# Optimization experiments

Measured on AMD Instinct MI355X. Metric: run time of the kernel, lower is better.

Reference implementation:

```python
import jax, jax.numpy as jnp
import numpy as np

T, B, I, H = 256, 128, 512, 1024

def setup_inputs() -> dict:
    key = jax.random.key(0)
    k1, k2, k3, k4, k5 = jax.random.split(key, 5)
    s_ih = 1.0 / np.sqrt(H)
    return {
        "x": jax.random.normal(k1, (T, B, I), dtype=jnp.float32),
        "hidden": jnp.zeros((B, H), dtype=jnp.float32),
        "W_ih": jax.random.uniform(k2, (H, I), jnp.float32, -s_ih, s_ih),
        "W_hh": jax.random.uniform(k3, (H, H), jnp.float32, -s_ih, s_ih),
        "b_ih": jax.random.uniform(k4, (H,), jnp.float32, -s_ih, s_ih),
        "b_hh": jax.random.uniform(k5, (H,), jnp.float32, -s_ih, s_ih),
    }

def reference(x, hidden, W_ih, W_hh, b_ih, b_hh):
    # Faithful to the source: forward() applies the RNNCell to the SAME
    # initial hidden at every timestep (hidden is never updated in the loop).
    # out[t] = relu(x[t] @ W_ih^T + b_ih + hidden @ W_hh^T + b_hh)
    h_term = hidden @ W_hh.T + b_hh          # (B, H), shared across time
    pre = jnp.einsum('tbi,hi->tbh', x, W_ih) + b_ih + h_term  # (T, B, H)
    out = jax.nn.relu(pre)
    return out, out[-1]
```

## Files before the change

### kernel.cpp

```cpp
#include <hip/hip_runtime.h>
#include <hip/hip_bf16.h>
#include <stdint.h>

#define T_DIM 256
#define B_DIM 128
#define I_DIM 512
#define H_DIM 1024
#define M_DIM (T_DIM * B_DIM)

typedef __attribute__((ext_vector_type(4))) float f32x4;
typedef __attribute__((ext_vector_type(8))) short short8;

__device__ inline unsigned short f2bf(float f) {
    __hip_bfloat16 h = __float2bfloat16(f);
    unsigned short u;
    __builtin_memcpy(&u, &h, sizeof(u));
    return u;
}

__device__ inline void gload_lds16(const void* g, void* l) {
    __builtin_amdgcn_global_load_lds(
        (const __attribute__((address_space(1))) uint32_t*)g,
        (__attribute__((address_space(3))) uint32_t*)l, 16, 0, 0);
}

__global__ void pack_W(const float* __restrict__ W, unsigned short* __restrict__ Wp) {
    int id = blockIdx.x * 256 + threadIdx.x;
    int s = id & 7;
    int r = (id >> 3) & 127;
    int kst = (id >> 10) & 7;
    int nt = id >> 13;
    int srcg = s ^ (r & 7);
    const float* src = W + (size_t)(nt * 128 + r) * I_DIM + kst * 64 + srcg * 8;
    f32x4 lo = *(const f32x4*)src;
    f32x4 hi = *(const f32x4*)(src + 4);
    union { unsigned short us[8]; short8 v; } pk;
#pragma unroll
    for (int j = 0; j < 4; ++j) { pk.us[j] = f2bf(lo[j]); pk.us[4 + j] = f2bf(hi[j]); }
    *(short8*)(Wp + (size_t)id * 8) = pk.v;
}

__global__ __launch_bounds__(256, 3) void gemm_main(
    const float* __restrict__ X, const unsigned short* __restrict__ Wp,
    const float* __restrict__ biasall, float* __restrict__ C,
    float* __restrict__ Clast) {
    __shared__ float Asf[128 * 64];
    __shared__ unsigned short Bsb[128 * 64];

    const int tid = threadIdx.x;
    const int lane = tid & 63;
    const int wid = tid >> 6;
    const int wr = wid >> 1, wc = wid & 1;
    const int llo = lane & 15, lhi = lane >> 4;

    const int orig = blockIdx.x;
    const int nwg = gridDim.x;
    const int wg = ((orig & 7) * (nwg >> 3)) + (orig >> 3);
    const int mt = wg >> 3;
    const int nt = wg & 7;
    const int m0 = mt * 128;
    const int n0 = nt * 128;

    const int arow_l = tid >> 4;
    const int csrc = (tid & 15) ^ arow_l;
    const float* Abase = X + (size_t)(m0 + arow_l) * I_DIM + csrc * 4;
    const unsigned short* Bbase = Wp + (size_t)nt * 8 * 8192 + (size_t)tid * 8;

    f32x4 acc[4][4] = {};

#pragma unroll
    for (int kst = 0; kst < I_DIM / 64; ++kst) {
        if (kst) __syncthreads();
        const float* asrc = Abase + kst * 64;
#pragma unroll
        for (int g = 0; g < 8; ++g)
            gload_lds16(asrc + (size_t)g * 16 * I_DIM,
                        (char*)Asf + (g * 256 + tid) * 16);
        const unsigned short* bsrc = Bbase + kst * 8192;
#pragma unroll
        for (int g = 0; g < 4; ++g)
            gload_lds16(bsrc + g * 2048, (char*)Bsb + (g * 256 + tid) * 16);
        __syncthreads();

#pragma unroll
        for (int ks = 0; ks < 2; ++ks) {
            short8 af[4], bfv[4];
#pragma unroll
            for (int mi = 0; mi < 4; ++mi) {
                int ar = wr * 64 + mi * 16 + llo;
                int g0 = ks * 8 + lhi * 2;
                f32x4 a0 = *(const f32x4*)&Asf[ar * 64 + ((g0 ^ (ar & 15)) << 2)];
                f32x4 a1 = *(const f32x4*)&Asf[ar * 64 + (((g0 + 1) ^ (ar & 15)) << 2)];
                union { unsigned short s[8]; short8 v; } pk;
#pragma unroll
                for (int j = 0; j < 4; ++j) {
                    pk.s[j] = f2bf(a0[j]);
                    pk.s[4 + j] = f2bf(a1[j]);
                }
                af[mi] = pk.v;
            }
#pragma unroll
            for (int ni = 0; ni < 4; ++ni) {
                int br = wc * 64 + ni * 16 + llo;
                int g = ks * 4 + lhi;
                bfv[ni] = *(const short8*)&Bsb[br * 64 + ((g ^ (br & 7)) << 3)];
            }
#pragma unroll
            for (int mi = 0; mi < 4; ++mi)
#pragma unroll
                for (int ni = 0; ni < 4; ++ni)
                    acc[mi][ni] = __builtin_amdgcn_mfma_f32_16x16x32_bf16(
                        af[mi], bfv[ni], acc[mi][ni], 0, 0, 0);
        }
    }

    const bool last_tile = (m0 == M_DIM - 128);
#pragma unroll
    for (int mi = 0; mi < 4; ++mi) {
#pragma unroll
        for (int ni = 0; ni < 4; ++ni) {
            int col = n0 + wc * 64 + ni * 16 + llo;
            int rowb = m0 + wr * 64 + mi * 16 + lhi * 4;
#pragma unroll
            for (int r = 0; r < 4; ++r) {
                int row = rowb + r;
                float v = acc[mi][ni][r] + biasall[(row & 127) * H_DIM + col];
                v = fmaxf(v, 0.0f);
                C[(size_t)row * H_DIM + col] = v;
                if (last_tile) Clast[(row & 127) * H_DIM + col] = v;
            }
        }
    }
}

template <int MODE>
__global__ __launch_bounds__(256, 2) void gemm_bt(
    const float* __restrict__ A, const float* __restrict__ Bm,
    int M, int N, int K,
    const float* __restrict__ bias0, const float* __restrict__ bias1,
    float* __restrict__ C, float* __restrict__ Clast) {
    __shared__ unsigned short As[128 * 64];
    __shared__ unsigned short Bs[128 * 64];

    const int tid = threadIdx.x;
    const int wid = tid >> 6;
    const int lane = tid & 63;
    const int wr = wid >> 1, wc = wid & 1;
    const int lhi = lane >> 4;
    const int llo = lane & 15;

    const int orig = blockIdx.x;
    const int nwg = gridDim.x;
    const int wg = (nwg > 8 && (nwg & 7) == 0)
                       ? ((orig & 7) * (nwg >> 3) + (orig >> 3))
                       : orig;
    const int m0 = (wg >> 3) * 128;
    const int n0 = (wg & 7) * 128;

    const int srow = tid >> 3;
    const int c8 = tid & 7;
    const int slot8 = (c8 ^ (srow & 7)) * 8;

    const float* Aptr = A + (size_t)(m0 + srow) * K + c8 * 8;
    const float* Bptr = Bm + (size_t)(n0 + srow) * K + c8 * 8;

    f32x4 pf[2][4][2];

    auto issue = [&](int k0) {
#pragma unroll
        for (int g = 0; g < 4; ++g) {
            const float* pa = Aptr + (size_t)g * 32 * K + k0;
            const float* pb = Bptr + (size_t)g * 32 * K + k0;
            pf[0][g][0] = *(const f32x4*)pa;
            pf[0][g][1] = *(const f32x4*)(pa + 4);
            pf[1][g][0] = *(const f32x4*)pb;
            pf[1][g][1] = *(const f32x4*)(pb + 4);
        }
    };
    auto write_lds = [&]() {
#pragma unroll
        for (int g = 0; g < 4; ++g) {
            union { unsigned short s[8]; short8 v; } pka, pkb;
#pragma unroll
            for (int j = 0; j < 4; ++j) {
                pka.s[j] = f2bf(pf[0][g][0][j]);
                pka.s[4 + j] = f2bf(pf[0][g][1][j]);
                pkb.s[j] = f2bf(pf[1][g][0][j]);
                pkb.s[4 + j] = f2bf(pf[1][g][1][j]);
            }
            *(short8*)&As[(srow + g * 32) * 64 + slot8] = pka.v;
            *(short8*)&Bs[(srow + g * 32) * 64 + slot8] = pkb.v;
        }
    };

    f32x4 acc[4][4] = {};

    auto compute = [&]() {
#pragma unroll
        for (int ks = 0; ks < 2; ++ks) {
            short8 af[4], bfr[4];
#pragma unroll
            for (int mi = 0; mi < 4; ++mi) {
                int ar = wr * 64 + mi * 16 + llo;
                int slot = ((ks << 2) + lhi) ^ (ar & 7);
                af[mi] = *(const short8*)&As[ar * 64 + slot * 8];
            }
#pragma unroll
            for (int ni = 0; ni < 4; ++ni) {
                int br = wc * 64 + ni * 16 + llo;
                int slot = ((ks << 2) + lhi) ^ (br & 7);
                bfr[ni] = *(const short8*)&Bs[br * 64 + slot * 8];
            }
#pragma unroll
            for (int mi = 0; mi < 4; ++mi)
#pragma unroll
                for (int ni = 0; ni < 4; ++ni)
                    acc[mi][ni] = __builtin_amdgcn_mfma_f32_16x16x32_bf16(
                        af[mi], bfr[ni], acc[mi][ni], 0, 0, 0);
        }
    };

    issue(0);
    write_lds();
    __syncthreads();
    for (int k0 = 64; k0 < K; k0 += 64) {
        issue(k0);
        compute();
        __syncthreads();
        write_lds();
        __syncthreads();
    }
    compute();

    const bool last_tile = (m0 == M - 128);
#pragma unroll
    for (int mi = 0; mi < 4; ++mi) {
#pragma unroll
        for (int ni = 0; ni < 4; ++ni) {
            int col = n0 + wc * 64 + ni * 16 + llo;
            int rowb = m0 + wr * 64 + mi * 16 + lhi * 4;
            if (MODE == 0) {
                float bsum = bias0[col] + bias1[col];
#pragma unroll
                for (int r = 0; r < 4; ++r)
                    C[(size_t)(rowb + r) * N + col] = acc[mi][ni][r] + bsum;
            } else {
#pragma unroll
                for (int r = 0; r < 4; ++r) {
                    int row = rowb + r;
                    float v = acc[mi][ni][r] + bias0[(row & 127) * N + col];
                    v = fmaxf(v, 0.0f);
                    C[(size_t)row * N + col] = v;
                    if (last_tile) Clast[(row & 127) * N + col] = v;
                }
            }
        }
    }
}

extern "C" void kernel_launch(void* const* d_in, const int* in_sizes, int n_in,
                              void* d_out, int out_size, void* d_ws, size_t ws_size,
                              hipStream_t stream) {
    const float* x = (const float*)d_in[0];
    const float* hidden = (const float*)d_in[1];
    const float* W_ih = (const float*)d_in[2];
    const float* W_hh = (const float*)d_in[3];
    const float* b_ih = (const float*)d_in[4];
    const float* b_hh = (const float*)d_in[5];

    float* out = (float*)d_out;
    float* out_last = out + (size_t)T_DIM * B_DIM * H_DIM;

    float* biasall = (float*)d_ws;
    unsigned short* Wp = (unsigned short*)((char*)d_ws + 512 * 1024);
    const size_t ws_need = 512 * 1024 + (size_t)H_DIM * I_DIM * 2;

    gemm_bt<0><<<dim3(H_DIM / 128), dim3(256), 0, stream>>>(
        hidden, W_hh, B_DIM, H_DIM, H_DIM, b_ih, b_hh, biasall, nullptr);

    if (ws_size >= ws_need) {
        pack_W<<<dim3(H_DIM * I_DIM / 8 / 256), dim3(256), 0, stream>>>(W_ih, Wp);
        gemm_main<<<dim3(M_DIM / 128 * (H_DIM / 128)), dim3(256), 0, stream>>>(
            x, Wp, biasall, out, out_last);
    } else {
        gemm_bt<1><<<dim3(M_DIM / 128 * (H_DIM / 128)), dim3(256), 0, stream>>>(
            x, W_ih, M_DIM, H_DIM, I_DIM, biasall, nullptr, out, out_last);
    }
}
```

Baseline: 109.9 us.

## Pre-pack X to swizzled bf16 and double-buffer LDS tiles in main GEMM

Adds a separate pass that converts the activation tensor x to bf16 in the same swizzled tile layout as the weights. The main GEMM then loads bf16 directly with no per-fragment fp32-to-bf16 conversion. The main loop now double-buffers A and B tiles in LDS, using explicit vmcnt waits and barriers so the next k-stage loads overlap compute. In exchange it adds a full extra read and write of x (about 32 MB in bf16) in a pre-pass, doubles LDS use, and lowers the launch-bounds occupancy hint from 3 to 2.

```diff
diff --git a/kernel.cpp b/kernel.cpp
--- a/kernel.cpp
+++ b/kernel.cpp
@@ -24,28 +24,29 @@
         (__attribute__((address_space(3))) uint32_t*)l, 16, 0, 0);
 }
 
-__global__ void pack_W(const float* __restrict__ W, unsigned short* __restrict__ Wp) {
+__global__ void pack_swz(const float* __restrict__ src,
+                         unsigned short* __restrict__ dst) {
     int id = blockIdx.x * 256 + threadIdx.x;
-    int s = id & 7;
-    int r = (id >> 3) & 127;
+    int slot = id & 7;
+    int row = (id >> 3) & 127;
     int kst = (id >> 10) & 7;
-    int nt = id >> 13;
-    int srcg = s ^ (r & 7);
-    const float* src = W + (size_t)(nt * 128 + r) * I_DIM + kst * 64 + srcg * 8;
-    f32x4 lo = *(const f32x4*)src;
-    f32x4 hi = *(const f32x4*)(src + 4);
+    int tile = id >> 13;
+    int g = slot ^ (row & 7);
+    const float* s = src + (size_t)(tile * 128 + row) * I_DIM + kst * 64 + g * 8;
+    f32x4 lo = *(const f32x4*)s;
+    f32x4 hi = *(const f32x4*)(s + 4);
     union { unsigned short us[8]; short8 v; } pk;
 #pragma unroll
     for (int j = 0; j < 4; ++j) { pk.us[j] = f2bf(lo[j]); pk.us[4 + j] = f2bf(hi[j]); }
-    *(short8*)(Wp + (size_t)id * 8) = pk.v;
-}
-
-__global__ __launch_bounds__(256, 3) void gemm_main(
-    const float* __restrict__ X, const unsigned short* __restrict__ Wp,
+    *(short8*)(dst + (size_t)id * 8) = pk.v;
+}
+
+__global__ __launch_bounds__(256, 2) void gemm_main(
+    const unsigned short* __restrict__ Xp, const unsigned short* __restrict__ Wp,
     const float* __restrict__ biasall, float* __restrict__ C,
     float* __restrict__ Clast) {
-    __shared__ float Asf[128 * 64];
-    __shared__ unsigned short Bsb[128 * 64];
+    __shared__ unsigned short As[2][128 * 64];
+    __shared__ unsigned short Bs[2][128 * 64];
 
     const int tid = threadIdx.x;
     const int lane = tid & 63;
@@ -54,56 +55,43 @@
     const int llo = lane & 15, lhi = lane >> 4;
 
     const int orig = blockIdx.x;
-    const int nwg = gridDim.x;
-    const int wg = ((orig & 7) * (nwg >> 3)) + (orig >> 3);
+    const int wg = ((orig & 7) * (2048 >> 3)) + (orig >> 3);
     const int mt = wg >> 3;
     const int nt = wg & 7;
     const int m0 = mt * 128;
     const int n0 = nt * 128;
 
-    const int arow_l = tid >> 4;
-    const int csrc = (tid & 15) ^ arow_l;
-    const float* Abase = X + (size_t)(m0 + arow_l) * I_DIM + csrc * 4;
-    const unsigned short* Bbase = Wp + (size_t)nt * 8 * 8192 + (size_t)tid * 8;
+    const unsigned short* Abase = Xp + (size_t)mt * 65536 + (size_t)tid * 8;
+    const unsigned short* Bbase = Wp + (size_t)nt * 65536 + (size_t)tid * 8;
+
+    auto stage = [&](int kst, int buf) {
+        const unsigned short* a = Abase + (size_t)kst * 8192;
+        const unsigned short* b = Bbase + (size_t)kst * 8192;
+#pragma unroll
+        for (int g = 0; g < 4; ++g)
+            gload_lds16(a + g * 2048, (char*)As[buf] + (g * 256 + tid) * 16);
+#pragma unroll
+        for (int g = 0; g < 4; ++g)
+            gload_lds16(b + g * 2048, (char*)Bs[buf] + (g * 256 + tid) * 16);
+    };
 
     f32x4 acc[4][4] = {};
 
-#pragma unroll
-    for (int kst = 0; kst < I_DIM / 64; ++kst) {
-        if (kst) __syncthreads();
-        const float* asrc = Abase + kst * 64;
-#pragma unroll
-        for (int g = 0; g < 8; ++g)
-            gload_lds16(asrc + (size_t)g * 16 * I_DIM,
-                        (char*)Asf + (g * 256 + tid) * 16);
-        const unsigned short* bsrc = Bbase + kst * 8192;
-#pragma unroll
-        for (int g = 0; g < 4; ++g)
-            gload_lds16(bsrc + g * 2048, (char*)Bsb + (g * 256 + tid) * 16);
-        __syncthreads();
-
+    auto compute = [&](int buf) {
 #pragma unroll
         for (int ks = 0; ks < 2; ++ks) {
             short8 af[4], bfv[4];
 #pragma unroll
             for (int mi = 0; mi < 4; ++mi) {
                 int ar = wr * 64 + mi * 16 + llo;
-                int g0 = ks * 8 + lhi * 2;
-                f32x4 a0 = *(const f32x4*)&Asf[ar * 64 + ((g0 ^ (ar & 15)) << 2)];
-                f32x4 a1 = *(const f32x4*)&Asf[ar * 64 + (((g0 + 1) ^ (ar & 15)) << 2)];
-                union { unsigned short s[8]; short8 v; } pk;
-#pragma unroll
-                for (int j = 0; j < 4; ++j) {
-                    pk.s[j] = f2bf(a0[j]);
-                    pk.s[4 + j] = f2bf(a1[j]);
-                }
-                af[mi] = pk.v;
+                int g = ks * 4 + lhi;
+                af[mi] = *(const short8*)&As[buf][ar * 64 + ((g ^ (ar & 7)) << 3)];
             }
 #pragma unroll
             for (int ni = 0; ni < 4; ++ni) {
                 int br = wc * 64 + ni * 16 + llo;
                 int g = ks * 4 + lhi;
-                bfv[ni] = *(const short8*)&Bsb[br * 64 + ((g ^ (br & 7)) << 3)];
+                bfv[ni] = *(const short8*)&Bs[buf][br * 64 + ((g ^ (br & 7)) << 3)];
             }
 #pragma unroll
             for (int mi = 0; mi < 4; ++mi)
@@ -112,6 +100,22 @@
                     acc[mi][ni] = __builtin_amdgcn_mfma_f32_16x16x32_bf16(
                         af[mi], bfv[ni], acc[mi][ni], 0, 0, 0);
         }
+    };
+
+    stage(0, 0);
+    stage(1, 1);
+#pragma unroll
+    for (int k = 0; k < 8; ++k) {
+        if (k < 7)
+            asm volatile("s_waitcnt vmcnt(8)" ::: "memory");
+        else
+            asm volatile("s_waitcnt vmcnt(0)" ::: "memory");
+        __builtin_amdgcn_s_barrier();
+        __builtin_amdgcn_sched_barrier(0);
+        compute(k & 1);
+        __builtin_amdgcn_sched_barrier(0);
+        __builtin_amdgcn_s_barrier();
+        if (k + 2 < 8) stage(k + 2, k & 1);
     }
 
     const bool last_tile = (m0 == M_DIM - 128);
@@ -273,15 +277,17 @@
 
     float* biasall = (float*)d_ws;
     unsigned short* Wp = (unsigned short*)((char*)d_ws + 512 * 1024);
-    const size_t ws_need = 512 * 1024 + (size_t)H_DIM * I_DIM * 2;
+    unsigned short* Xp = (unsigned short*)((char*)d_ws + 1536 * 1024);
+    const size_t ws_need = 1536 * 1024 + (size_t)M_DIM * I_DIM * 2;
 
     gemm_bt<0><<<dim3(H_DIM / 128), dim3(256), 0, stream>>>(
         hidden, W_hh, B_DIM, H_DIM, H_DIM, b_ih, b_hh, biasall, nullptr);
 
     if (ws_size >= ws_need) {
-        pack_W<<<dim3(H_DIM * I_DIM / 8 / 256), dim3(256), 0, stream>>>(W_ih, Wp);
+        pack_swz<<<dim3(M_DIM * I_DIM / 8 / 256), dim3(256), 0, stream>>>(x, Xp);
+        pack_swz<<<dim3(H_DIM * I_DIM / 8 / 256), dim3(256), 0, stream>>>(W_ih, Wp);
         gemm_main<<<dim3(M_DIM / 128 * (H_DIM / 128)), dim3(256), 0, stream>>>(
-            x, Wp, biasall, out, out_last);
+            Xp, Wp, biasall, out, out_last);
     } else {
         gemm_bt<1><<<dim3(M_DIM / 128 * (H_DIM / 128)), dim3(256), 0, stream>>>(
             x, W_ih, M_DIM, H_DIM, I_DIM, biasall, nullptr, out, out_last);
```

Measured after the change: 132.6 us. 20.6% more time.
